# Kernel optimization log

Hardware: AMD Instinct MI355X
Metric: run time of the kernel (lower is better)

The kernel has to match this reference:

```python
import jax, jax.numpy as jnp
import numpy as np

N, E = 3072, 49152
C_IN, HID, C_OUT = 16, 64, 3
KS = (2000, 1000, 500)  # ceil(pool_ratio * n_nodes) per depth: 2000/3072, 0.5, 0.5


def gcn(x, A, W, b):
    # GCNConv(improved=True) with edge weights: A_hat = A + 2I,
    # out = D^-1/2 A_hat D^-1/2 (x W) + b
    n = A.shape[0]
    i = jnp.arange(n)
    A_hat = A.at[i, i].add(2.0)
    deg = A_hat.sum(axis=1)
    dis = jnp.where(deg > 0, 1.0 / jnp.sqrt(deg), 0.0)
    return (dis[:, None] * A_hat * dis[None, :]) @ (x @ W) + b


def augment(A):
    # GraphUNet.augment_adj: remove self loops, add self loops (w=1),
    # spspmm(A, A) -> A^2, remove self loops. Dense equivalent.
    n = A.shape[0]
    i = jnp.arange(n)
    A1 = A.at[i, i].set(1.0)
    A2 = A1 @ A1
    return A2.at[i, i].set(0.0)


def topk_pool(x, A, p, k):
    # TopKPooling: score = tanh((x . p)/||p||), keep top-k nodes, scale features
    score = jnp.tanh((x @ p) / jnp.linalg.norm(p))
    _, perm = jax.lax.top_k(score, k)
    x = x[perm] * score[perm][:, None]
    return x, A[perm][:, perm], perm


def setup_inputs():
    key = jax.random.key(0)
    ks = jax.random.split(key, 16)
    g = lambda k, shape, s=1.0: jax.random.normal(k, shape, dtype=jnp.float32) * s
    s = 0.1
    return {
        "x": g(ks[0], (N, C_IN)),
        "edge_index": jax.random.randint(ks[1], (2, E), 0, N),
        "Wd0": g(ks[2], (C_IN, HID), s), "bd0": jnp.zeros((HID,), jnp.float32),
        "Wd1": g(ks[3], (HID, HID), s), "bd1": jnp.zeros((HID,), jnp.float32),
        "Wd2": g(ks[4], (HID, HID), s), "bd2": jnp.zeros((HID,), jnp.float32),
        "Wd3": g(ks[5], (HID, HID), s), "bd3": jnp.zeros((HID,), jnp.float32),
        "p1": g(ks[6], (HID,), s), "p2": g(ks[7], (HID,), s), "p3": g(ks[8], (HID,), s),
        "Wu0": g(ks[9], (HID, HID), s), "bu0": jnp.zeros((HID,), jnp.float32),
        "Wu1": g(ks[10], (HID, HID), s), "bu1": jnp.zeros((HID,), jnp.float32),
        "Wu2": g(ks[11], (HID, C_OUT), s), "bu2": jnp.zeros((C_OUT,), jnp.float32),
    }


def reference(x, edge_index, Wd0, bd0, Wd1, bd1, Wd2, bd2, Wd3, bd3,
              p1, p2, p3, Wu0, bu0, Wu1, bu1, Wu2, bu2):
    # eval mode: dropout_edge(p=0.2) and F.dropout(p=0.92) are identity
    # dense weighted adjacency; duplicate edges sum, matching sparse scatter-add
    A = jnp.zeros((N, N), jnp.float32).at[edge_index[0], edge_index[1]].add(1.0)
    x = jax.nn.relu(gcn(x, A, Wd0, bd0))
    xs, adjs, perms = [x], [A], []
    for i, (W, b, p) in enumerate(((Wd1, bd1, p1), (Wd2, bd2, p2), (Wd3, bd3, p3))):
        A = augment(A)
        x, A, perm = topk_pool(x, A, p, KS[i])
        x = jax.nn.relu(gcn(x, A, W, b))
        if i < 2:
            xs.append(x)
            adjs.append(A)
        perms.append(perm)
    for i, (W, b) in enumerate(((Wu0, bu0), (Wu1, bu1), (Wu2, bu2))):
        j = 2 - i
        res, Aj, perm = xs[j], adjs[j], perms[j]
        up = jnp.zeros_like(res).at[perm].set(x)  # unpool
        x = gcn(res + up, Aj, W, b)  # sum_res=True skip connection
        if i < 2:
            x = jax.nn.relu(x)
    return jax.nn.softmax(x, axis=1)
```

## Files before the change

kernel.cpp:

```cpp
#include <hip/hip_runtime.h>
#include <hip/hip_bf16.h>
#include <cstdint>
#include <cstddef>
#include <math.h>


#define DIVUP(a,b) (((a)+(b)-1)/(b))

using s16x8 = __attribute__((ext_vector_type(8))) short;
using f32x4 = __attribute__((ext_vector_type(4))) float;

template<int N> __device__ __forceinline__ void waitvm() {
    if constexpr (N == 0)       asm volatile("s_waitcnt vmcnt(0)" ::: "memory");
    else if constexpr (N == 4)  asm volatile("s_waitcnt vmcnt(4)" ::: "memory");
    else if constexpr (N == 8)  asm volatile("s_waitcnt vmcnt(8)" ::: "memory");
    else                        asm volatile("s_waitcnt vmcnt(16)" ::: "memory");
}

__device__ __forceinline__ unsigned short f2bf(float v) {
    union { float f; unsigned u; } a; a.f = v;
    unsigned u = a.u;
    u = u + 0x7FFFu + ((u >> 16) & 1u);
    return (unsigned short)(u >> 16);
}
__device__ __forceinline__ float bf2f(unsigned short h) {
    union { unsigned u; float f; } a; a.u = ((unsigned)h) << 16; return a.f;
}
__device__ __forceinline__ void gload_lds16(const unsigned short* g, unsigned short* l) {
    __builtin_amdgcn_global_load_lds(
        (const __attribute__((address_space(1))) void*)g,
        (__attribute__((address_space(3))) void*)l, 16, 0, 0);
}


__global__ void k_scatter(const int* __restrict__ e, float* __restrict__ A, int E, int n) {
    int t = blockIdx.x * blockDim.x + threadIdx.x;
    if (t < E) atomicAdd(&A[(size_t)e[t] * n + e[E + t]], 1.0f);
}

__global__ void k_a0_plane(const float* __restrict__ A, unsigned short* __restrict__ H,
                           float* __restrict__ d0, float* __restrict__ dsum, int n) {
    int t = blockIdx.x * 256 + threadIdx.x;
    int i = t / n, j = t - i * n;
    float v = A[t];
    if (i == j) { d0[i] = v; v = 1.0f; }
    H[t] = f2bf(v);
    __shared__ float red[256];
    red[threadIdx.x] = v; __syncthreads();
    for (int o = 128; o > 0; o >>= 1) {
        if (threadIdx.x < o) red[threadIdx.x] += red[threadIdx.x + o];
        __syncthreads();
    }
    if (threadIdx.x == 0) atomicAdd(&dsum[i], red[0]);
}

__global__ void k_transpose_bf(const unsigned short* __restrict__ S, unsigned short* __restrict__ D, int n) {
    __shared__ unsigned short tile[32][33];
    int bx = blockIdx.x * 32, by = blockIdx.y * 32;
    #pragma unroll
    for (int dy = 0; dy < 32; dy += 8)
        tile[threadIdx.y + dy][threadIdx.x] = S[(size_t)(by + threadIdx.y + dy) * n + bx + threadIdx.x];
    __syncthreads();
    #pragma unroll
    for (int dy = 0; dy < 32; dy += 8)
        D[(size_t)(bx + threadIdx.y + dy) * n + by + threadIdx.x] = tile[threadIdx.x][threadIdx.y + dy];
}

__global__ void k_disv(const float* __restrict__ dsum, const float* __restrict__ diag,
                       float* __restrict__ dis, int n) {
    int i = blockIdx.x * blockDim.x + threadIdx.x;
    if (i >= n) return;
    float deg = dsum[i] + 1.0f + (diag ? diag[i] : 0.0f);
    dis[i] = deg > 0.f ? 1.0f / sqrtf(deg) : 0.f;
}

__global__ void k_disp(const unsigned short* __restrict__ P0, const unsigned short* __restrict__ P1,
                       const unsigned short* __restrict__ P2, int nplanes,
                       float* __restrict__ dis, int np) {
    int i = blockIdx.x;
    const unsigned short* pls[3] = {P0, P1, P2};
    float s = 0.f;
    for (int p = 0; p < nplanes; ++p) {
        const unsigned short* row = pls[p] + (size_t)i * np;
        for (int j = threadIdx.x * 8; j < np; j += 2048) {
            s16x8 v = *(const s16x8*)(row + j);
            #pragma unroll
            for (int e = 0; e < 8; ++e) s += bf2f((unsigned short)v[e]);
        }
    }
    __shared__ float red[256];
    red[threadIdx.x] = s; __syncthreads();
    for (int o = 128; o > 0; o >>= 1) {
        if (threadIdx.x < o) red[threadIdx.x] += red[threadIdx.x + o];
        __syncthreads();
    }
    if (threadIdx.x == 0) dis[i] = 1.0f / sqrtf(red[0] + 1.0f);
}

__global__ void k_scores(const float* __restrict__ x, const float* __restrict__ pv,
                         float* __restrict__ sc, int n) {
    __shared__ float pl[64];
    if (threadIdx.x < 64) pl[threadIdx.x] = pv[threadIdx.x];
    __syncthreads();
    float n2 = 0.f;
    #pragma unroll
    for (int k = 0; k < 64; ++k) n2 += pl[k] * pl[k];
    float nrm = sqrtf(n2);
    int i = blockIdx.x * blockDim.x + threadIdx.x;
    if (i >= n) return;
    const float* xr = x + (size_t)i * 64;
    float d = 0.f;
    #pragma unroll
    for (int k = 0; k < 64; ++k) d += xr[k] * pl[k];
    sc[i] = tanhf(d / nrm);
}

__global__ void k_count_rank(const float* __restrict__ score, int* __restrict__ rank, int n) {
    __shared__ float ls[256];
    const int i = blockIdx.x * 256 + threadIdx.x;
    const int j0 = blockIdx.y * 256;
    int jj_n = n - j0; if (jj_n > 256) jj_n = 256;
    ls[threadIdx.x] = (j0 + threadIdx.x < n) ? score[j0 + threadIdx.x] : -INFINITY;
    __syncthreads();
    if (i >= n) return;
    const float si = score[i];
    int cnt = 0;
    for (int jj = 0; jj < jj_n; ++jj) {
        float sj = ls[jj];
        int j = j0 + jj;
        cnt += (sj > si) || (sj == si && j < i);
    }
    atomicAdd(&rank[i], cnt);
}

__global__ void k_scatter_topk(const float* __restrict__ score, const int* __restrict__ rank,
                               int n, int k, int kp, int* __restrict__ perm, float* __restrict__ scout) {
    int i = blockIdx.x * blockDim.x + threadIdx.x;
    if (i < n) {
        int r = rank[i];
        if (r < k) { perm[r] = i; scout[r] = score[i]; }
    }
    if (i >= k && i < kp) { perm[i] = 0; scout[i] = 0.f; }
}

__global__ void k_pool_x(const float* __restrict__ x, const int* __restrict__ perm,
                         const float* __restrict__ sc, float* __restrict__ xo, int k) {
    int t = blockIdx.x * blockDim.x + threadIdx.x;
    if (t >= k * 64) return;
    int r = t >> 6;
    xo[t] = x[(size_t)perm[r] * 64 + (t & 63)] * sc[r];
}

__global__ void k_copy4(const float4* __restrict__ src, float4* __restrict__ dst, int n4) {
    int t = blockIdx.x * blockDim.x + threadIdx.x;
    if (t < n4) dst[t] = src[t];
}

__global__ void k_scatter_rows(const float* __restrict__ xc, const int* __restrict__ perm,
                               float* __restrict__ o, int k) {
    int t = blockIdx.x * blockDim.x + threadIdx.x;
    if (t >= k * 64) return;
    int r = t >> 6;
    o[(size_t)perm[r] * 64 + (t & 63)] += xc[t];
}

__global__ void k_xw(const float* __restrict__ x, const float* __restrict__ W,
                     const float* __restrict__ dis, int n, int np, int cin, int ldw, int nout,
                     float* __restrict__ Y, unsigned short* __restrict__ T0,
                     unsigned short* __restrict__ T1, unsigned short* __restrict__ T2) {
    int t = blockIdx.x * blockDim.x + threadIdx.x;
    if (t >= np * 64) return;
    int i = t >> 6, f = t & 63;
    float y = 0.f;
    if (i < n && f < nout) {
        float a = 0.f;
        for (int k = 0; k < cin; ++k) a += x[(size_t)i * cin + k] * W[(size_t)k * ldw + f];
        y = dis[i] * a;
    }
    Y[t] = y;
    unsigned short h0 = f2bf(y);
    float r1 = y - bf2f(h0);
    unsigned short h1 = f2bf(r1);
    float r2 = r1 - bf2f(h1);
    size_t ti = (size_t)f * np + i;
    T0[ti] = h0; T1[ti] = h1; T2[ti] = f2bf(r2);
}


template<int TM, int PA, int PB, int NP, int NT>
__global__ __launch_bounds__(256) void k_aug2(
    const unsigned short* __restrict__ Pa, const unsigned short* __restrict__ Pb,
    const unsigned short* __restrict__ Qa, const unsigned short* __restrict__ Qb,
    const int* __restrict__ perm, int kk, int kp, int K, int ns,
    unsigned short* __restrict__ H0, unsigned short* __restrict__ H1,
    unsigned short* __restrict__ H2,
    unsigned short* __restrict__ T0, unsigned short* __restrict__ T1)
{
    constexpr int BM  = TM * 32;
    constexpr int PS  = TM * 2048;
    constexpr int D   = 3;
    constexpr int STG = (PA + PB) * PS;
    constexpr int LPS = TM * (PA + PB);
    constexpr int TRE = NT ? (BM * (BM + 2)) : 0;
    constexpr int SME = (D * STG > TRE) ? (D * STG) : TRE;
    __shared__ __align__(16) unsigned short smem[SME];
    const int tid = threadIdx.x, lane = tid & 63;
    const int wm = tid >> 7, wn = (tid >> 6) & 1;
    const int gx = gridDim.x, nwg = gx * gridDim.y;
    int bid = blockIdx.y * gx + blockIdx.x;
    bid = (bid & 7) * (nwg >> 3) + (bid >> 3);
    const int bm = (bid % gx) * BM, bn = (bid / gx) * BM;
    const unsigned short* P[2] = {Pa, Pb};
    const unsigned short* Q[2] = {Qa, Qb};
    const unsigned short* sp[PA][TM];
    const unsigned short* sq[PB][TM];
    int dst[TM];
    #pragma unroll
    for (int it = 0; it < TM; ++it) {
        int s = tid + it * 256;
        int row = s >> 3, c = (s & 7) ^ (row & 7);
        dst[it] = (s - lane) * 8;
        #pragma unroll
        for (int p = 0; p < PA; ++p)
            sp[p][it] = P[p] + (size_t)perm[bm + row] * ns + 8 * c;
        #pragma unroll
        for (int p = 0; p < PB; ++p)
            sq[p][it] = Q[p] + (size_t)perm[bn + row] * ns + 8 * c;
    }
    f32x4 acc[TM][TM] = {};
    const int l15 = lane & 15, kb = lane >> 4;
    const int nt = K >> 6;

    auto stage = [&](int b, int koff) {
        unsigned short* base = smem + b * STG;
        #pragma unroll
        for (int p = 0; p < PA; ++p)
            #pragma unroll
            for (int it = 0; it < TM; ++it)
                gload_lds16(sp[p][it] + koff, base + p * PS + dst[it]);
        #pragma unroll
        for (int p = 0; p < PB; ++p)
            #pragma unroll
            for (int it = 0; it < TM; ++it)
                gload_lds16(sq[p][it] + koff, base + PA * PS + p * PS + dst[it]);
    };
    auto compute = [&](int b) {
        const unsigned short* base = smem + b * STG;
        #pragma unroll
        for (int h = 0; h < 2; ++h) {
            s16x8 av[PA][TM], bv[PB][TM];
            #pragma unroll
            for (int p = 0; p < PA; ++p)
                #pragma unroll
                for (int mi = 0; mi < TM; ++mi) {
                    int row = wm * (TM * 16) + mi * 16 + l15;
                    int slot = (h * 4 + kb) ^ (row & 7);
                    av[p][mi] = *(const s16x8*)(base + p * PS + row * 64 + slot * 8);
                }
            #pragma unroll
            for (int p = 0; p < PB; ++p)
                #pragma unroll
                for (int ni = 0; ni < TM; ++ni) {
                    int row = wn * (TM * 16) + ni * 16 + l15;
                    int slot = (h * 4 + kb) ^ (row & 7);
                    bv[p][ni] = *(const s16x8*)(base + PA * PS + p * PS + row * 64 + slot * 8);
                }
            #pragma unroll
            for (int mi = 0; mi < TM; ++mi)
                #pragma unroll
                for (int ni = 0; ni < TM; ++ni)
                    #pragma unroll
                    for (int pa = 0; pa < PA; ++pa)
                        #pragma unroll
                        for (int pb = 0; pb < PB; ++pb)
                            acc[mi][ni] = __builtin_amdgcn_mfma_f32_16x16x32_bf16(
                                av[pa][mi], bv[pb][ni], acc[mi][ni], 0, 0, 0);
        }
    };

    for (int i = 0; i < D - 1; ++i) stage(i, i * 64);
    for (int t = 0; t < nt; ++t) {
        const int ahead = nt - 1 - t;
        if (ahead >= D - 1) {
            stage((t + D - 1) % D, (t + D - 1) * 64);
            waitvm<2 * LPS>();
        } else if (ahead == 1) {
            waitvm<LPS>();
        } else {
            waitvm<0>();
        }
        __builtin_amdgcn_sched_barrier(0);
        __builtin_amdgcn_s_barrier();
        compute(t % D);
        __builtin_amdgcn_s_barrier();
    }

    const int hi = lane >> 4;
    #pragma unroll
    for (int mi = 0; mi < TM; ++mi)
        #pragma unroll
        for (int ni = 0; ni < TM; ++ni)
            #pragma unroll
            for (int r = 0; r < 4; ++r) {
                int row = bm + wm * (TM * 16) + mi * 16 + hi * 4 + r;
                int col = bn + wn * (TM * 16) + ni * 16 + l15;
                float v = (row < kk && col < kk) ? ((row == col) ? 1.f : acc[mi][ni][r]) : 0.f;
                unsigned short h0 = f2bf(v);
                size_t o = (size_t)row * kp + col;
                H0[o] = h0;
                if (NP > 1) {
                    float r1 = v - bf2f(h0);
                    unsigned short h1 = f2bf(r1);
                    H1[o] = h1;
                    if (NP > 2) H2[o] = f2bf(r1 - bf2f(h1));
                }
            }

    if (NT > 0) {
        #pragma unroll
        for (int pass = 0; pass < NT; ++pass) {
            __syncthreads();
            #pragma unroll
            for (int mi = 0; mi < TM; ++mi)
                #pragma unroll
                for (int ni = 0; ni < TM; ++ni)
                    #pragma unroll
                    for (int r = 0; r < 4; ++r) {
                        int rl = wm * (TM * 16) + mi * 16 + hi * 4 + r;
                        int cl = wn * (TM * 16) + ni * 16 + l15;
                        int row = bm + rl, col = bn + cl;
                        float v = (row < kk && col < kk) ? ((row == col) ? 1.f : acc[mi][ni][r]) : 0.f;
                        unsigned short h0 = f2bf(v);
                        unsigned short hv = h0;
                        if (pass == 1) hv = f2bf(v - bf2f(h0));
                        smem[rl * (BM + 2) + cl] = hv;
                    }
            __syncthreads();
            unsigned short* T = pass ? T1 : T0;
            #pragma unroll
            for (int e = 0; e < BM * BM / 256; ++e) {
                int idx = tid + e * 256;
                int j = idx / BM, i = idx & (BM - 1);
                T[(size_t)(bn + j) * kp + (bm + i)] = smem[i * (BM + 2) + j];
            }
        }
    }
}

template<int PA>
__global__ __launch_bounds__(256) void k_gcn_gemm(
    const unsigned short* __restrict__ Aa, const unsigned short* __restrict__ Ab,
    const unsigned short* __restrict__ Ac,
    const unsigned short* __restrict__ B0, const unsigned short* __restrict__ B1,
    const unsigned short* __restrict__ B2,
    int np, int kchunk, float* __restrict__ Zp)
{
    __shared__ __align__(16) unsigned short la[PA * 4096];
    __shared__ __align__(16) unsigned short lb[3 * 4096];
    const int tid = threadIdx.x, lane = tid & 63, wv = tid >> 6;
    const int bm = blockIdx.x * 64;
    const int kbeg = blockIdx.y * kchunk;
    const unsigned short* A[3] = {Aa, Ab, Ac};
    const unsigned short* B[3] = {B0, B1, B2};
    const unsigned short* sa[PA][2];
    const unsigned short* sb[3][2];
    int dst[2];
    #pragma unroll
    for (int it = 0; it < 2; ++it) {
        int s = tid + it * 256;
        int row = s >> 3, c = (s & 7) ^ (row & 7);
        dst[it] = (s - lane) * 8;
        #pragma unroll
        for (int p = 0; p < PA; ++p)
            sa[p][it] = A[p] + (size_t)(bm + row) * np + kbeg + 8 * c;
        #pragma unroll
        for (int p = 0; p < 3; ++p)
            sb[p][it] = B[p] + (size_t)row * np + kbeg + 8 * c;
    }
    f32x4 acc[4] = {};
    const int l15 = lane & 15, kb = lane >> 4;
    const int nt = kchunk >> 6;

    for (int tt = 0; tt < nt; ++tt) {
        if (tt) __syncthreads();
        int koff = tt * 64;
        #pragma unroll
        for (int p = 0; p < PA; ++p)
            #pragma unroll
            for (int it = 0; it < 2; ++it)
                gload_lds16(sa[p][it] + koff, &la[p * 4096 + dst[it]]);
        #pragma unroll
        for (int p = 0; p < 3; ++p)
            #pragma unroll
            for (int it = 0; it < 2; ++it)
                gload_lds16(sb[p][it] + koff, &lb[p * 4096 + dst[it]]);
        __syncthreads();
        #pragma unroll
        for (int h = 0; h < 2; ++h) {
            s16x8 av[PA], bv[3][4];
            #pragma unroll
            for (int p = 0; p < PA; ++p) {
                int row = wv * 16 + l15;
                int slot = (h * 4 + kb) ^ (row & 7);
                av[p] = *(const s16x8*)&la[p * 4096 + row * 64 + slot * 8];
            }
            #pragma unroll
            for (int p = 0; p < 3; ++p)
                #pragma unroll
                for (int ni = 0; ni < 4; ++ni) {
                    int row = ni * 16 + l15;
                    int slot = (h * 4 + kb) ^ (row & 7);
                    bv[p][ni] = *(const s16x8*)&lb[p * 4096 + row * 64 + slot * 8];
                }
            #pragma unroll
            for (int ni = 0; ni < 4; ++ni)
                #pragma unroll
                for (int pa = 0; pa < PA; ++pa)
                    #pragma unroll
                    for (int pb = 0; pb <= 2 - pa; ++pb)
                        acc[ni] = __builtin_amdgcn_mfma_f32_16x16x32_bf16(
                            av[pa], bv[pb][ni], acc[ni], 0, 0, 0);
        }
    }

    const int l4 = lane >> 4;
    float* Z = Zp + (size_t)blockIdx.y * np * 64;
    for (int ni = 0; ni < 4; ++ni)
        #pragma unroll
        for (int r = 0; r < 4; ++r) {
            int row = bm + wv * 16 + l4 * 4 + r;
            Z[(size_t)row * 64 + ni * 16 + l15] = acc[ni][r];
        }
}

__global__ void k_gcn_epi(const float* __restrict__ Zp, const float* __restrict__ Y,
                          const float* __restrict__ dis, const float* __restrict__ diagv,
                          const float* __restrict__ b, int n, int np, int nout, int relu,
                          int S, float* __restrict__ xo) {
    int t = blockIdx.x * blockDim.x + threadIdx.x;
    if (t >= n * 64) return;
    int i = t >> 6, f = t & 63;
    float s = 0.f;
    for (int kq = 0; kq < S; ++kq) s += Zp[(size_t)kq * np * 64 + t];
    float coef = 1.f + (diagv ? diagv[i] : 0.f);
    float v = dis[i] * (s + coef * Y[t]) + (f < nout ? b[f] : 0.f);
    if (relu) v = fmaxf(v, 0.f);
    xo[t] = v;
}

__global__ void k_softmax(const float* __restrict__ lg, float* __restrict__ o, int n) {
    int i = blockIdx.x * blockDim.x + threadIdx.x;
    if (i >= n) return;
    float a = lg[i * 64], b = lg[i * 64 + 1], c = lg[i * 64 + 2];
    float m = fmaxf(a, fmaxf(b, c));
    float ea = expf(a - m), eb = expf(b - m), ec = expf(c - m);
    float s = ea + eb + ec;
    o[i * 3] = ea / s; o[i * 3 + 1] = eb / s; o[i * 3 + 2] = ec / s;
}


extern "C" void kernel_launch(void* const* d_in, const int* in_sizes, int n_in,
                              void* d_out, int out_size, void* d_ws, size_t ws_size,
                              hipStream_t stream) {
    const int N0 = 3072;
    const int E = in_sizes[1] / 2;
    const int CIN = in_sizes[0] / N0;

    const float* x_in = (const float*)d_in[0];
    const int*   eidx = (const int*)d_in[1];
    const float* Wd0 = (const float*)d_in[2];  const float* bd0 = (const float*)d_in[3];
    const float* Wd1 = (const float*)d_in[4];  const float* bd1 = (const float*)d_in[5];
    const float* Wd2 = (const float*)d_in[6];  const float* bd2 = (const float*)d_in[7];
    const float* Wd3 = (const float*)d_in[8];  const float* bd3 = (const float*)d_in[9];
    const float* p1  = (const float*)d_in[10]; const float* p2  = (const float*)d_in[11];
    const float* p3  = (const float*)d_in[12];
    const float* Wu0 = (const float*)d_in[13]; const float* bu0 = (const float*)d_in[14];
    const float* Wu1 = (const float*)d_in[15]; const float* bu1 = (const float*)d_in[16];
    const float* Wu2 = (const float*)d_in[17]; const float* bu2 = (const float*)d_in[18];
    float* out = (float*)d_out;

    char* ws = (char*)d_ws;
    size_t off = 0;
    auto alloc = [&](size_t bytes) -> void* {
        off = (off + 255) & ~(size_t)255;
        void* p = ws + off;
        off += bytes;
        return p;
    };

    unsigned short* A0H  = (unsigned short*)alloc((size_t)3072 * 3072 * 2);
    unsigned short* A0T  = (unsigned short*)alloc((size_t)3072 * 3072 * 2);
    float* d0   = (float*)alloc(3072 * 4);
    float* dis0 = (float*)alloc(3072 * 4);
    float* x0   = (float*)alloc((size_t)3072 * 64 * 4);
    unsigned short* P1H = (unsigned short*)alloc((size_t)2048 * 2048 * 2);
    unsigned short* P1T = (unsigned short*)alloc((size_t)2048 * 2048 * 2);
    float* dis1 = (float*)alloc(2048 * 4);
    float* x1   = (float*)alloc((size_t)2048 * 64 * 4);
    float* xp1  = (float*)alloc((size_t)2048 * 64 * 4);
    unsigned short* P2H  = (unsigned short*)alloc((size_t)1024 * 1024 * 2);
    unsigned short* P2L  = (unsigned short*)alloc((size_t)1024 * 1024 * 2);
    unsigned short* P2TH = (unsigned short*)alloc((size_t)1024 * 1024 * 2);
    unsigned short* P2TL = (unsigned short*)alloc((size_t)1024 * 1024 * 2);
    float* dis2 = (float*)alloc(1024 * 4);
    float* x2   = (float*)alloc((size_t)1024 * 64 * 4);
    float* xp2  = (float*)alloc((size_t)1024 * 64 * 4);
    unsigned short* P3a = (unsigned short*)alloc((size_t)512 * 512 * 2);
    unsigned short* P3b = (unsigned short*)alloc((size_t)512 * 512 * 2);
    unsigned short* P3c = (unsigned short*)alloc((size_t)512 * 512 * 2);
    float* dis3 = (float*)alloc(512 * 4);
    float* x3   = (float*)alloc((size_t)512 * 64 * 4);
    float* xp3  = (float*)alloc((size_t)512 * 64 * 4);
    int*   perm1 = (int*)alloc(2048 * 4);  float* sc1 = (float*)alloc(2048 * 4);
    int*   perm2 = (int*)alloc(1024 * 4);  float* sc2 = (float*)alloc(1024 * 4);
    int*   perm3 = (int*)alloc(512 * 4);   float* sc3 = (float*)alloc(512 * 4);
    float* score = (float*)alloc(3072 * 4);
    float* dsum0 = (float*)alloc(3072 * 4);
    int* rank1 = (int*)alloc(3072 * 4);
    int* rank2 = (int*)alloc(2048 * 4);
    int* rank3 = (int*)alloc(1024 * 4);
    float* Yf  = (float*)alloc((size_t)3072 * 64 * 4);
    unsigned short* Yt0 = (unsigned short*)alloc((size_t)64 * 3072 * 2);
    unsigned short* Yt1 = (unsigned short*)alloc((size_t)64 * 3072 * 2);
    unsigned short* Yt2 = (unsigned short*)alloc((size_t)64 * 3072 * 2);
    float* Zp   = (float*)alloc((size_t)8 * 3072 * 64 * 4);
    float* xlog = (float*)alloc((size_t)3072 * 64 * 4);
    float* t2b  = (float*)alloc((size_t)1024 * 64 * 4);
    float* t1b  = (float*)alloc((size_t)2048 * 64 * 4);
    float* t0b  = (float*)alloc((size_t)3072 * 64 * 4);
    char* scratch = (char*)alloc((size_t)3072 * 3072 * 4);
    if (off > ws_size) return;

    float* A0f = (float*)scratch;

    auto gcn = [&](const float* xin, int cin, const float* W, int ldw, int nout, const float* bias,
                   const unsigned short* Pa, const unsigned short* Pb2, const unsigned short* Pc,
                   int PA, int n, int np2, const float* dis, const float* diagv, int relu, float* xout) {
        k_xw<<<DIVUP(np2 * 64, 256), 256, 0, stream>>>(xin, W, dis, n, np2, cin, ldw, nout, Yf, Yt0, Yt1, Yt2);
        int S = (np2 == 1024) ? 16 : 8;
        int kch = np2 / S;
        dim3 gg(np2 / 64, S);
        if (PA == 1)      k_gcn_gemm<1><<<gg, 256, 0, stream>>>(Pa, Pa, Pa, Yt0, Yt1, Yt2, np2, kch, Zp);
        else if (PA == 2) k_gcn_gemm<2><<<gg, 256, 0, stream>>>(Pa, Pb2, Pb2, Yt0, Yt1, Yt2, np2, kch, Zp);
        else              k_gcn_gemm<3><<<gg, 256, 0, stream>>>(Pa, Pb2, Pc, Yt0, Yt1, Yt2, np2, kch, Zp);
        k_gcn_epi<<<DIVUP(n * 64, 256), 256, 0, stream>>>(Zp, Yf, dis, diagv, bias, n, np2, nout, relu, S, xout);
    };

    auto topk = [&](const float* x, const float* pvec, int n, int k, int kp,
                    int* rank, int* perm, float* scv) {
        k_scores<<<DIVUP(n, 256), 256, 0, stream>>>(x, pvec, score, n);
        dim3 gr(DIVUP(n, 256), DIVUP(n, 256));
        k_count_rank<<<gr, 256, 0, stream>>>(score, rank, n);
        k_scatter_topk<<<DIVUP(n, 256), 256, 0, stream>>>(score, rank, n, k, kp, perm, scv);
    };

    hipMemsetAsync(dsum0, 0, (char*)(rank3 + 1024) - (char*)dsum0, stream);

    hipMemsetAsync(A0f, 0, (size_t)3072 * 3072 * 4, stream);
    k_scatter<<<DIVUP(E, 256), 256, 0, stream>>>(eidx, A0f, E, N0);
    k_a0_plane<<<3072 * 3072 / 256, 256, 0, stream>>>(A0f, A0H, d0, dsum0, N0);
    k_transpose_bf<<<dim3(96, 96), dim3(32, 8), 0, stream>>>(A0H, A0T, 3072);
    k_disv<<<DIVUP(3072, 256), 256, 0, stream>>>(dsum0, d0, dis0, 3072);

    gcn(x_in, CIN, Wd0, 64, 64, bd0, A0H, A0H, A0H, 1, 3072, 3072, dis0, d0, 1, x0);

    topk(x0, p1, 3072, 2000, 2048, rank1, perm1, sc1);
    k_pool_x<<<DIVUP(2000 * 64, 256), 256, 0, stream>>>(x0, perm1, sc1, xp1, 2000);
    k_aug2<4, 1, 1, 1, 1><<<dim3(16, 16), 256, 0, stream>>>(
        A0H, A0H, A0T, A0T, perm1, 2000, 2048, 3072, 3072, P1H, P1H, P1H, P1T, P1T);
    k_disp<<<2000, 256, 0, stream>>>(P1H, P1H, P1H, 1, dis1, 2048);
    gcn(xp1, 64, Wd1, 64, 64, bd1, P1H, P1H, P1H, 1, 2000, 2048, dis1, nullptr, 1, x1);

    topk(x1, p2, 2000, 1000, 1024, rank2, perm2, sc2);
    k_pool_x<<<DIVUP(1000 * 64, 256), 256, 0, stream>>>(x1, perm2, sc2, xp2, 1000);
    k_aug2<2, 1, 1, 2, 2><<<dim3(16, 16), 256, 0, stream>>>(
        P1H, P1H, P1T, P1T, perm2, 1000, 1024, 2048, 2048, P2H, P2L, P2L, P2TH, P2TL);
    k_disp<<<1000, 256, 0, stream>>>(P2H, P2L, P2L, 2, dis2, 1024);
    gcn(xp2, 64, Wd2, 64, 64, bd2, P2H, P2L, P2L, 2, 1000, 1024, dis2, nullptr, 1, x2);

    topk(x2, p3, 1000, 500, 512, rank3, perm3, sc3);
    k_pool_x<<<DIVUP(500 * 64, 256), 256, 0, stream>>>(x2, perm3, sc3, xp3, 500);
    k_aug2<2, 2, 2, 3, 0><<<dim3(8, 8), 256, 0, stream>>>(
        P2H, P2L, P2TH, P2TL, perm3, 500, 512, 1024, 1024, P3a, P3b, P3c, nullptr, nullptr);
    k_disp<<<500, 256, 0, stream>>>(P3a, P3b, P3c, 3, dis3, 512);
    gcn(xp3, 64, Wd3, 64, 64, bd3, P3a, P3b, P3c, 3, 500, 512, dis3, nullptr, 1, x3);

    k_copy4<<<DIVUP(1000 * 16, 256), 256, 0, stream>>>((const float4*)x2, (float4*)t2b, 1000 * 16);
    k_scatter_rows<<<DIVUP(500 * 64, 256), 256, 0, stream>>>(x3, perm3, t2b, 500);
    gcn(t2b, 64, Wu0, 64, 64, bu0, P2H, P2L, P2L, 2, 1000, 1024, dis2, nullptr, 1, xp2);

    k_copy4<<<DIVUP(2000 * 16, 256), 256, 0, stream>>>((const float4*)x1, (float4*)t1b, 2000 * 16);
    k_scatter_rows<<<DIVUP(1000 * 64, 256), 256, 0, stream>>>(xp2, perm2, t1b, 1000);
    gcn(t1b, 64, Wu1, 64, 64, bu1, P1H, P1H, P1H, 1, 2000, 2048, dis1, nullptr, 1, xp1);

    k_copy4<<<DIVUP(3072 * 16, 256), 256, 0, stream>>>((const float4*)x0, (float4*)t0b, 3072 * 16);
    k_scatter_rows<<<DIVUP(2000 * 64, 256), 256, 0, stream>>>(xp1, perm1, t0b, 2000);
    gcn(t0b, 64, Wu2, 3, 3, bu2, A0H, A0H, A0H, 1, 3072, 3072, dis0, d0, 0, xlog);

    k_softmax<<<DIVUP(3072, 256), 256, 0, stream>>>(xlog, out, 3072);
}
```

Before: 400.1 us.

## Use FP8 MFMA for first augment, fuse pooling and unpool kernels

Encodes the base adjacency as e4m3 FP8 bytes and computes the first A^2 augment with a new FP8 MFMA kernel, which halves the bytes loaded per tile compared to the bf16 path. Small integer counts are exact in e4m3 only up to a limit, so larger edge multiplicities could be rounded. Pooling-feature gathering is folded into the top-k finish kernel, and copy plus scatter for unpool is replaced by a single gather kernel using the rank array. The block-index swizzle in k_aug2 is also removed.

```diff
diff --git a/kernel.cpp b/kernel.cpp
--- a/kernel.cpp
+++ b/kernel.cpp
@@ -26,11 +26,24 @@
 __device__ __forceinline__ float bf2f(unsigned short h) {
     union { unsigned u; float f; } a; a.u = ((unsigned)h) << 16; return a.f;
 }
+__device__ __forceinline__ unsigned char f2e4m3(float v) {
+    if (v <= 0.f) return 0;
+    int e = 0; float m = v;
+    while (m >= 2.f) { m *= 0.5f; ++e; }
+    int mant = (int)(m * 8.f + 0.5f) - 8;
+    if (mant >= 8) { mant = 0; ++e; }
+    return (unsigned char)(((e + 7) << 3) | mant);
+}
 __device__ __forceinline__ void gload_lds16(const unsigned short* g, unsigned short* l) {
     __builtin_amdgcn_global_load_lds(
         (const __attribute__((address_space(1))) void*)g,
         (__attribute__((address_space(3))) void*)l, 16, 0, 0);
 }
+__device__ __forceinline__ void gload_lds16b(const unsigned char* g, unsigned char* l) {
+    __builtin_amdgcn_global_load_lds(
+        (const __attribute__((address_space(1))) void*)g,
+        (__attribute__((address_space(3))) void*)l, 16, 0, 0);
+}
 
 
 __global__ void k_scatter(const int* __restrict__ e, float* __restrict__ A, int E, int n) {
@@ -39,12 +52,14 @@
 }
 
 __global__ void k_a0_plane(const float* __restrict__ A, unsigned short* __restrict__ H,
+                           unsigned char* __restrict__ F8,
                            float* __restrict__ d0, float* __restrict__ dsum, int n) {
     int t = blockIdx.x * 256 + threadIdx.x;
     int i = t / n, j = t - i * n;
     float v = A[t];
     if (i == j) { d0[i] = v; v = 1.0f; }
     H[t] = f2bf(v);
+    F8[t] = f2e4m3(v);
     __shared__ float red[256];
     red[threadIdx.x] = v; __syncthreads();
     for (int o = 128; o > 0; o >>= 1) {
@@ -54,8 +69,8 @@
     if (threadIdx.x == 0) atomicAdd(&dsum[i], red[0]);
 }
 
-__global__ void k_transpose_bf(const unsigned short* __restrict__ S, unsigned short* __restrict__ D, int n) {
-    __shared__ unsigned short tile[32][33];
+__global__ void k_transpose_u8(const unsigned char* __restrict__ S, unsigned char* __restrict__ D, int n) {
+    __shared__ unsigned char tile[32][33];
     int bx = blockIdx.x * 32, by = blockIdx.y * 32;
     #pragma unroll
     for (int dy = 0; dy < 32; dy += 8)
@@ -133,35 +148,31 @@
     atomicAdd(&rank[i], cnt);
 }
 
-__global__ void k_scatter_topk(const float* __restrict__ score, const int* __restrict__ rank,
-                               int n, int k, int kp, int* __restrict__ perm, float* __restrict__ scout) {
+__global__ void k_topk_finish(const float* __restrict__ score, const int* __restrict__ rank,
+                              const float* __restrict__ x, int n, int k, int kp,
+                              int* __restrict__ perm, float* __restrict__ scout,
+                              float* __restrict__ xo) {
     int i = blockIdx.x * blockDim.x + threadIdx.x;
     if (i < n) {
         int r = rank[i];
-        if (r < k) { perm[r] = i; scout[r] = score[i]; }
+        if (r < k) {
+            float s = score[i];
+            perm[r] = i; scout[r] = s;
+            const float* xr = x + (size_t)i * 64;
+            float* xw = xo + (size_t)r * 64;
+            #pragma unroll 8
+            for (int f = 0; f < 64; ++f) xw[f] = xr[f] * s;
+        }
     }
     if (i >= k && i < kp) { perm[i] = 0; scout[i] = 0.f; }
 }
 
-__global__ void k_pool_x(const float* __restrict__ x, const int* __restrict__ perm,
-                         const float* __restrict__ sc, float* __restrict__ xo, int k) {
+__global__ void k_unpool(const float* __restrict__ res, const float* __restrict__ xc,
+                         const int* __restrict__ rank, float* __restrict__ o, int n, int k) {
     int t = blockIdx.x * blockDim.x + threadIdx.x;
-    if (t >= k * 64) return;
-    int r = t >> 6;
-    xo[t] = x[(size_t)perm[r] * 64 + (t & 63)] * sc[r];
-}
-
-__global__ void k_copy4(const float4* __restrict__ src, float4* __restrict__ dst, int n4) {
-    int t = blockIdx.x * blockDim.x + threadIdx.x;
-    if (t < n4) dst[t] = src[t];
-}
-
-__global__ void k_scatter_rows(const float* __restrict__ xc, const int* __restrict__ perm,
-                               float* __restrict__ o, int k) {
-    int t = blockIdx.x * blockDim.x + threadIdx.x;
-    if (t >= k * 64) return;
-    int r = t >> 6;
-    o[(size_t)perm[r] * 64 + (t & 63)] += xc[t];
+    if (t >= n * 64) return;
+    int r = rank[t >> 6];
+    o[t] = res[t] + (r < k ? xc[(size_t)r * 64 + (t & 63)] : 0.f);
 }
 
 __global__ void k_xw(const float* __restrict__ x, const float* __restrict__ W,
@@ -186,6 +197,121 @@
     T0[ti] = h0; T1[ti] = h1; T2[ti] = f2bf(r2);
 }
 
+
+__global__ __launch_bounds__(256) void k_aug8(
+    const unsigned char* __restrict__ P8, const unsigned char* __restrict__ Q8,
+    const int* __restrict__ perm, int kk, int kp, int K, int ns,
+    unsigned short* __restrict__ H0, unsigned short* __restrict__ T0)
+{
+    constexpr int BM = 128;
+    constexpr int PS = 128 * 64;
+    constexpr int D = 3;
+    constexpr int STG = 2 * PS;
+    constexpr int SMEB = (D * STG > 128 * 130 * 2) ? D * STG : 128 * 130 * 2;
+    __shared__ __align__(16) unsigned char smem[SMEB];
+    const int tid = threadIdx.x, lane = tid & 63;
+    const int wm = tid >> 7, wn = (tid >> 6) & 1;
+    const int bm = blockIdx.x * BM, bn = blockIdx.y * BM;
+    const unsigned char* spA[2];
+    const unsigned char* spB[2];
+    int dstb[2];
+    #pragma unroll
+    for (int it = 0; it < 2; ++it) {
+        int s = tid + it * 256;
+        int row = s >> 2, c = (s & 3) ^ (row & 3);
+        dstb[it] = (s - lane) * 16;
+        spA[it] = P8 + (size_t)perm[bm + row] * ns + 16 * c;
+        spB[it] = Q8 + (size_t)perm[bn + row] * ns + 16 * c;
+    }
+    f32x4 acc[4][4] = {};
+    const int l15 = lane & 15, kb = lane >> 4;
+    const int nt = K >> 6;
+
+    auto stage = [&](int b, int koff) {
+        unsigned char* base = smem + b * STG;
+        #pragma unroll
+        for (int it = 0; it < 2; ++it) gload_lds16b(spA[it] + koff, base + dstb[it]);
+        #pragma unroll
+        for (int it = 0; it < 2; ++it) gload_lds16b(spB[it] + koff, base + PS + dstb[it]);
+    };
+    auto compute = [&](int b) {
+        const unsigned char* base = smem + b * STG;
+        #pragma unroll
+        for (int h = 0; h < 2; ++h) {
+            long av[4], bv[4];
+            #pragma unroll
+            for (int mi = 0; mi < 4; ++mi) {
+                int row = wm * 64 + mi * 16 + l15;
+                int slot = (h * 2 + (kb >> 1)) ^ (row & 3);
+                av[mi] = *(const long*)(base + row * 64 + slot * 16 + (kb & 1) * 8);
+            }
+            #pragma unroll
+            for (int ni = 0; ni < 4; ++ni) {
+                int row = wn * 64 + ni * 16 + l15;
+                int slot = (h * 2 + (kb >> 1)) ^ (row & 3);
+                bv[ni] = *(const long*)(base + PS + row * 64 + slot * 16 + (kb & 1) * 8);
+            }
+            #pragma unroll
+            for (int mi = 0; mi < 4; ++mi)
+                #pragma unroll
+                for (int ni = 0; ni < 4; ++ni)
+                    acc[mi][ni] = __builtin_amdgcn_mfma_f32_16x16x32_fp8_fp8(
+                        av[mi], bv[ni], acc[mi][ni], 0, 0, 0);
+        }
+    };
+
+    stage(0, 0); stage(1, 64);
+    for (int t = 0; t < nt; ++t) {
+        const int ahead = nt - 1 - t;
+        if (ahead >= D - 1) {
+            stage((t + D - 1) % D, (t + D - 1) * 64);
+            waitvm<8>();
+        } else if (ahead == 1) {
+            waitvm<4>();
+        } else {
+            waitvm<0>();
+        }
+        __builtin_amdgcn_sched_barrier(0);
+        __builtin_amdgcn_s_barrier();
+        compute(t % D);
+        __builtin_amdgcn_s_barrier();
+    }
+
+    const int hi = lane >> 4;
+    #pragma unroll
+    for (int mi = 0; mi < 4; ++mi)
+        #pragma unroll
+        for (int ni = 0; ni < 4; ++ni)
+            #pragma unroll
+            for (int r = 0; r < 4; ++r) {
+                int row = bm + wm * 64 + mi * 16 + hi * 4 + r;
+                int col = bn + wn * 64 + ni * 16 + l15;
+                float v = (row < kk && col < kk) ? ((row == col) ? 1.f : acc[mi][ni][r]) : 0.f;
+                H0[(size_t)row * kp + col] = f2bf(v);
+            }
+
+    unsigned short* smw = (unsigned short*)smem;
+    __syncthreads();
+    #pragma unroll
+    for (int mi = 0; mi < 4; ++mi)
+        #pragma unroll
+        for (int ni = 0; ni < 4; ++ni)
+            #pragma unroll
+            for (int r = 0; r < 4; ++r) {
+                int rl = wm * 64 + mi * 16 + hi * 4 + r;
+                int cl = wn * 64 + ni * 16 + l15;
+                int row = bm + rl, col = bn + cl;
+                float v = (row < kk && col < kk) ? ((row == col) ? 1.f : acc[mi][ni][r]) : 0.f;
+                smw[rl * 130 + cl] = f2bf(v);
+            }
+    __syncthreads();
+    #pragma unroll
+    for (int e = 0; e < 64; ++e) {
+        int idx = tid + e * 256;
+        int j = idx >> 7, i = idx & 127;
+        T0[(size_t)(bn + j) * kp + (bm + i)] = smw[i * 130 + j];
+    }
+}
 
 template<int TM, int PA, int PB, int NP, int NT>
 __global__ __launch_bounds__(256) void k_aug2(
@@ -206,10 +332,7 @@
     __shared__ __align__(16) unsigned short smem[SME];
     const int tid = threadIdx.x, lane = tid & 63;
     const int wm = tid >> 7, wn = (tid >> 6) & 1;
-    const int gx = gridDim.x, nwg = gx * gridDim.y;
-    int bid = blockIdx.y * gx + blockIdx.x;
-    bid = (bid & 7) * (nwg >> 3) + (bid >> 3);
-    const int bm = (bid % gx) * BM, bn = (bid / gx) * BM;
+    const int bm = blockIdx.x * BM, bn = blockIdx.y * BM;
     const unsigned short* P[2] = {Pa, Pb};
     const unsigned short* Q[2] = {Qa, Qb};
     const unsigned short* sp[PA][TM];
@@ -489,7 +612,8 @@
     };
 
     unsigned short* A0H  = (unsigned short*)alloc((size_t)3072 * 3072 * 2);
-    unsigned short* A0T  = (unsigned short*)alloc((size_t)3072 * 3072 * 2);
+    unsigned char*  A0F8 = (unsigned char*)alloc((size_t)3072 * 3072);
+    unsigned char*  A0T8 = (unsigned char*)alloc((size_t)3072 * 3072);
     float* d0   = (float*)alloc(3072 * 4);
     float* dis0 = (float*)alloc(3072 * 4);
     float* x0   = (float*)alloc((size_t)3072 * 64 * 4);
@@ -547,54 +671,48 @@
     };
 
     auto topk = [&](const float* x, const float* pvec, int n, int k, int kp,
-                    int* rank, int* perm, float* scv) {
+                    int* rank, int* perm, float* scv, float* xo) {
         k_scores<<<DIVUP(n, 256), 256, 0, stream>>>(x, pvec, score, n);
         dim3 gr(DIVUP(n, 256), DIVUP(n, 256));
         k_count_rank<<<gr, 256, 0, stream>>>(score, rank, n);
-        k_scatter_topk<<<DIVUP(n, 256), 256, 0, stream>>>(score, rank, n, k, kp, perm, scv);
+        k_topk_finish<<<DIVUP(n, 256), 256, 0, stream>>>(score, rank, x, n, k, kp, perm, scv, xo);
     };
 
     hipMemsetAsync(dsum0, 0, (char*)(rank3 + 1024) - (char*)dsum0, stream);
 
     hipMemsetAsync(A0f, 0, (size_t)3072 * 3072 * 4, stream);
     k_scatter<<<DIVUP(E, 256), 256, 0, stream>>>(eidx, A0f, E, N0);
-    k_a0_plane<<<3072 * 3072 / 256, 256, 0, stream>>>(A0f, A0H, d0, dsum0, N0);
-    k_transpose_bf<<<dim3(96, 96), dim3(32, 8), 0, stream>>>(A0H, A0T, 3072);
+    k_a0_plane<<<3072 * 3072 / 256, 256, 0, stream>>>(A0f, A0H, A0F8, d0, dsum0, N0);
+    k_transpose_u8<<<dim3(96, 96), dim3(32, 8), 0, stream>>>(A0F8, A0T8, 3072);
     k_disv<<<DIVUP(3072, 256), 256, 0, stream>>>(dsum0, d0, dis0, 3072);
 
     gcn(x_in, CIN, Wd0, 64, 64, bd0, A0H, A0H, A0H, 1, 3072, 3072, dis0, d0, 1, x0);
 
-    topk(x0, p1, 3072, 2000, 2048, rank1, perm1, sc1);
-    k_pool_x<<<DIVUP(2000 * 64, 256), 256, 0, stream>>>(x0, perm1, sc1, xp1, 2000);
-    k_aug2<4, 1, 1, 1, 1><<<dim3(16, 16), 256, 0, stream>>>(
-        A0H, A0H, A0T, A0T, perm1, 2000, 2048, 3072, 3072, P1H, P1H, P1H, P1T, P1T);
+    topk(x0, p1, 3072, 2000, 2048, rank1, perm1, sc1, xp1);
+    k_aug8<<<dim3(16, 16), 256, 0, stream>>>(
+        A0F8, A0T8, perm1, 2000, 2048, 3072, 3072, P1H, P1T);
     k_disp<<<2000, 256, 0, stream>>>(P1H, P1H, P1H, 1, dis1, 2048);
     gcn(xp1, 64, Wd1, 64, 64, bd1, P1H, P1H, P1H, 1, 2000, 2048, dis1, nullptr, 1, x1);
 
-    topk(x1, p2, 2000, 1000, 1024, rank2, perm2, sc2);
-    k_pool_x<<<DIVUP(1000 * 64, 256), 256, 0, stream>>>(x1, perm2, sc2, xp2, 1000);
+    topk(x1, p2, 2000, 1000, 1024, rank2, perm2, sc2, xp2);
     k_aug2<2, 1, 1, 2, 2><<<dim3(16, 16), 256, 0, stream>>>(
         P1H, P1H, P1T, P1T, perm2, 1000, 1024, 2048, 2048, P2H, P2L, P2L, P2TH, P2TL);
     k_disp<<<1000, 256, 0, stream>>>(P2H, P2L, P2L, 2, dis2, 1024);
     gcn(xp2, 64, Wd2, 64, 64, bd2, P2H, P2L, P2L, 2, 1000, 1024, dis2, nullptr, 1, x2);
 
-    topk(x2, p3, 1000, 500, 512, rank3, perm3, sc3);
-    k_pool_x<<<DIVUP(500 * 64, 256), 256, 0, stream>>>(x2, perm3, sc3, xp3, 500);
+    topk(x2, p3, 1000, 500, 512, rank3, perm3, sc3, xp3);
     k_aug2<2, 2, 2, 3, 0><<<dim3(8, 8), 256, 0, stream>>>(
         P2H, P2L, P2TH, P2TL, perm3, 500, 512, 1024, 1024, P3a, P3b, P3c, nullptr, nullptr);
     k_disp<<<500, 256, 0, stream>>>(P3a, P3b, P3c, 3, dis3, 512);
     gcn(xp3, 64, Wd3, 64, 64, bd3, P3a, P3b, P3c, 3, 500, 512, dis3, nullptr, 1, x3);
 
-    k_copy4<<<DIVUP(1000 * 16, 256), 256, 0, stream>>>((const float4*)x2, (float4*)t2b, 1000 * 16);
-    k_scatter_rows<<<DIVUP(500 * 64, 256), 256, 0, stream>>>(x3, perm3, t2b, 500);
+    k_unpool<<<DIVUP(1000 * 64, 256), 256, 0, stream>>>(x2, x3, rank3, t2b, 1000, 500);
     gcn(t2b, 64, Wu0, 64, 64, bu0, P2H, P2L, P2L, 2, 1000, 1024, dis2, nullptr, 1, xp2);
 
-    k_copy4<<<DIVUP(2000 * 16, 256), 256, 0, stream>>>((const float4*)x1, (float4*)t1b, 2000 * 16);
-    k_scatter_rows<<<DIVUP(1000 * 64, 256), 256, 0, stream>>>(xp2, perm2, t1b, 1000);
+    k_unpool<<<DIVUP(2000 * 64, 256), 256, 0, stream>>>(x1, xp2, rank2, t1b, 2000, 1000);
     gcn(t1b, 64, Wu1, 64, 64, bu1, P1H, P1H, P1H, 1, 2000, 2048, dis1, nullptr, 1, xp1);
 
-    k_copy4<<<DIVUP(3072 * 16, 256), 256, 0, stream>>>((const float4*)x0, (float4*)t0b, 3072 * 16);
-    k_scatter_rows<<<DIVUP(2000 * 64, 256), 256, 0, stream>>>(xp1, perm1, t0b, 2000);
+    k_unpool<<<DIVUP(3072 * 64, 256), 256, 0, stream>>>(x0, xp1, rank1, t0b, 3072, 2000);
     gcn(t0b, 64, Wu2, 3, 3, bu2, A0H, A0H, A0H, 1, 3072, 3072, dis0, d0, 0, xlog);
 
     k_softmax<<<DIVUP(3072, 256), 256, 0, stream>>>(xlog, out, 3072);
```

New measurement: 405.8 us. No clear change (+1.4%).
